# Optimization experiments

Measured on AMD Instinct MI355X. Metric: run time of the kernel, lower is better.

The kernel has to match this reference:

```python
import jax, jax.numpy as jnp
import numpy as np

N, E, FE, H, G, L, OUT = 50000, 300000, 64, 256, 256, 4, 128
BN_EPS = 1e-5


def setup_inputs() -> dict:
    key = jax.random.key(0)
    ks = jax.random.split(key, 12)
    s = 0.05
    return dict(
        x=jax.random.normal(ks[0], (N, H), jnp.float32),
        edge_index=jax.random.randint(ks[1], (2, E), 0, N, dtype=jnp.int64),
        edge_attr=jax.random.normal(ks[2], (E, FE), jnp.float32),
        batch=jnp.sort(jax.random.randint(ks[3], (N,), 0, G, dtype=jnp.int64)),
        bond_W1=jax.random.normal(ks[4], (L, FE, H), jnp.float32) * s,
        bond_b1=jnp.zeros((L, H), jnp.float32),
        bond_W2=jax.random.normal(ks[5], (L, H, H), jnp.float32) * s,
        bond_b2=jnp.zeros((L, H), jnp.float32),
        mlp_W1=jax.random.normal(ks[6], (L, H, H), jnp.float32) * s,
        mlp_b1=jnp.zeros((L, H), jnp.float32),
        mlp_W2=jax.random.normal(ks[7], (L, H, H), jnp.float32) * s,
        mlp_b2=jnp.zeros((L, H), jnp.float32),
        eps=jnp.zeros((L,), jnp.float32),
        bn_gamma=jnp.ones((L, H), jnp.float32),
        bn_beta=jnp.zeros((L, H), jnp.float32),
        fc1_W=jax.random.normal(ks[8], (L * H, H), jnp.float32) * s,
        fc1_b=jnp.zeros((H,), jnp.float32),
        fc4_W=jax.random.normal(ks[9], (H, OUT), jnp.float32) * s,
        fc4_b=jnp.zeros((OUT,), jnp.float32),
    )


def reference(x, edge_index, edge_attr, batch,
              bond_W1, bond_b1, bond_W2, bond_b2,
              mlp_W1, mlp_b1, mlp_W2, mlp_b2,
              eps, bn_gamma, bn_beta,
              fc1_W, fc1_b, fc4_W, fc4_b):
    src, dst = edge_index[0], edge_index[1]  # x_j gathered from src, scatter-add to dst
    x_lst = []
    for l in range(L):
        # bond encoder: Linear -> ReLU -> Linear on edge features [E, FE] -> [E, H]
        e = jax.nn.relu(edge_attr @ bond_W1[l] + bond_b1[l]) @ bond_W2[l] + bond_b2[l]
        # message = relu(x_j + e), aggregate = scatter-add over destination nodes
        msg = jax.nn.relu(x[src] + e)  # [E, H]
        aggr = jax.ops.segment_sum(msg, dst, num_segments=N)  # [N, H]
        h = (1.0 + eps[l]) * x + aggr
        h = jax.nn.relu(h @ mlp_W1[l] + mlp_b1[l]) @ mlp_W2[l] + mlp_b2[l]
        h = jax.nn.relu(h)
        # BatchNorm over the node dimension (training-style batch statistics)
        mu = jnp.mean(h, axis=0)
        var = jnp.var(h, axis=0)
        x = (h - mu) * jax.lax.rsqrt(var + BN_EPS) * bn_gamma[l] + bn_beta[l]
        x_lst.append(x)
    xc = jnp.concatenate(x_lst, axis=-1)  # [N, L*H]
    # global mean pool over graphs
    sums = jax.ops.segment_sum(xc, batch, num_segments=G)  # [G, L*H]
    cnts = jax.ops.segment_sum(jnp.ones((N,), xc.dtype), batch, num_segments=G)
    pooled = sums / jnp.maximum(cnts, 1.0)[:, None]
    h = jax.nn.relu(pooled @ fc1_W + fc1_b)
    # dropout p=0.5 in eval mode -> identity
    return h @ fc4_W + fc4_b  # [G, OUT]
```

## Files before the change

### kernel.cpp

```cpp
#include <hip/hip_runtime.h>

#define NN 50000
#define NE 300000
#define FEA 64
#define HD 256
#define NG 256
#define NL 4
#define OD 128
#define SCB ((NN + 255) / 256)

typedef unsigned short u16;
typedef unsigned int u32;
typedef __attribute__((ext_vector_type(8))) short short8;
typedef __attribute__((ext_vector_type(4))) short s16x4;
typedef __attribute__((ext_vector_type(4))) float f32x4;

__device__ __forceinline__ u16 f2h(float f) {
    union { _Float16 h; u16 u; } v; v.h = (_Float16)f; return v.u;
}
__device__ __forceinline__ float h2f(u16 u) {
    union { u16 u; _Float16 h; } v; v.u = u; return (float)v.h;
}

typedef const __attribute__((address_space(1))) unsigned int gas_u32;
typedef __attribute__((address_space(3))) unsigned int las_u32;
__device__ __forceinline__ void gld16(const void* g, void* l) {
    __builtin_amdgcn_global_load_lds((gas_u32*)g, (las_u32*)l, 16, 0, 0);
}

__global__ __launch_bounds__(256, 2) void edge_k(
    const u16* __restrict__ eattrS, const u16* __restrict__ W1t,
    const float* __restrict__ bb1, const u16* __restrict__ W2t,
    const float* __restrict__ bb2,
    const int* __restrict__ srcI, const int* __restrict__ dstI,
    const u16* __restrict__ xh, float* __restrict__ aggr)
{
    __shared__ __align__(16) u16 bufW[256 * 64];
    __shared__ __align__(16) u16 bufT[64 * 256];
    __shared__ int srcL[64];
    const int tid = threadIdx.x;
    const int lane = tid & 63;
    const int w = tid >> 6;
    const int q = lane >> 4, c15 = lane & 15;
    const int e0 = blockIdx.x * 64;
    const int wb = tid & ~63;

    if (tid < 64) {
        int er = e0 + tid;
        int erc = er < NE ? er : NE - 1;
        srcL[tid] = srcI[erc];
    }
#pragma unroll
    for (int it = 0; it < 2; ++it) {
        const int i = it * 256 + tid;
        const int m = i >> 3, kb = i & 7;
        int row = e0 + m; if (row > NE - 1) row = NE - 1;
        gld16(eattrS + (size_t)row * FEA + ((kb ^ (m & 7)) * 8),
              &bufT[(it * 256 + wb) * 8]);
    }
#pragma unroll
    for (int it = 0; it < 8; ++it) {
        const int i = it * 256 + tid;
        const int n = i >> 3, kb = i & 7;
        gld16(W1t + (size_t)n * FEA + ((kb ^ (n & 7)) * 8),
              &bufW[(it * 256 + wb) * 8]);
    }
    __syncthreads();

    f32x4 acc1[4][4];
#pragma unroll
    for (int i = 0; i < 4; ++i)
#pragma unroll
        for (int j = 0; j < 4; ++j) acc1[i][j] = (f32x4)0.0f;
#pragma unroll
    for (int s = 0; s < 2; ++s) {
        short8 af[4], bf[4];
#pragma unroll
        for (int t = 0; t < 4; ++t) {
            const int kga = s * 4 + q;
            const int mm = t * 16 + c15;
            af[t] = *(const short8*)&bufT[mm * 64 + ((kga ^ (mm & 7)) * 8)];
            const int nn = w * 64 + t * 16 + c15;
            bf[t] = *(const short8*)&bufW[nn * 64 + ((kga ^ (nn & 7)) * 8)];
        }
        __builtin_amdgcn_s_setprio(1);
#pragma unroll
        for (int tm = 0; tm < 4; ++tm)
#pragma unroll
            for (int tn = 0; tn < 4; ++tn)
                acc1[tm][tn] = __builtin_amdgcn_mfma_f32_16x16x32_f16(
                    bf[tm], af[tn], acc1[tm][tn], 0, 0, 0);
        __builtin_amdgcn_s_setprio(0);
    }
    __syncthreads();

    auto stageW2 = [&](int cc) {
        const int k0c = cc * 32;
        const int hB = (cc & 1) * 1024;
#pragma unroll
        for (int it = 0; it < 4; ++it) {
            const int i = it * 256 + tid;
            const int n = i >> 2, j = i & 3;
            gld16(W2t + (size_t)n * HD + k0c + ((j ^ ((n >> 1) & 3)) * 8),
                  &bufW[(hB + it * 256 + wb) * 8]);
        }
    };
    stageW2(0);

    {
#pragma unroll
        for (int tm = 0; tm < 4; ++tm) {
            const float4 b1v = *(const float4*)(bb1 + w * 64 + tm * 16 + q * 4);
            const int kb = w * 8 + tm * 2 + (q >> 1);
#pragma unroll
            for (int tn = 0; tn < 4; ++tn) {
                const int edge = tn * 16 + c15;
                s16x4 o;
#pragma unroll
                for (int r = 0; r < 4; ++r) {
                    float v = acc1[tm][tn][r] + ((const float*)&b1v)[r];
                    v = v > 0.0f ? v : 0.0f;
                    o[r] = (short)f2h(v);
                }
                *(s16x4*)((char*)bufT + edge * 512 +
                          ((kb ^ (edge & 7)) << 4) + ((q & 1) << 3)) = o;
            }
        }
    }
    __syncthreads();

    f32x4 acc2[4][4];
#pragma unroll
    for (int i = 0; i < 4; ++i)
#pragma unroll
        for (int j = 0; j < 4; ++j) acc2[i][j] = (f32x4)0.0f;
#pragma unroll
    for (int c = 0; c < 8; ++c) {
        if (c < 7) {
            stageW2(c + 1);
        } else {
#pragma unroll
            for (int it = 0; it < 4; ++it) {
                const int i = it * 256 + tid;
                const int row = i >> 5, ch = i & 31;
                gld16(xh + (size_t)srcL[row] * HD + ch * 8,
                      &bufW[(it * 256 + wb) * 8]);
            }
        }
        short8 af[4], bf[4];
        const u16* hp = &bufW[(c & 1) * 8192];
#pragma unroll
        for (int t = 0; t < 4; ++t) {
            const int mm = t * 16 + c15;
            const int kbg = c * 4 + q;
            af[t] = *(const short8*)&bufT[mm * 256 + ((kbg ^ (mm & 7)) * 8)];
            const int nn = w * 64 + t * 16 + c15;
            bf[t] = *(const short8*)&hp[nn * 32 + ((q ^ ((nn >> 1) & 3)) * 8)];
        }
        __builtin_amdgcn_s_setprio(1);
#pragma unroll
        for (int tm = 0; tm < 4; ++tm)
#pragma unroll
            for (int tn = 0; tn < 4; ++tn)
                acc2[tm][tn] = __builtin_amdgcn_mfma_f32_16x16x32_f16(
                    af[tm], bf[tn], acc2[tm][tn], 0, 0, 0);
        __builtin_amdgcn_s_setprio(0);
        __syncthreads();
    }

#pragma unroll
    for (int it = 0; it < 4; ++it) {
        const int i = 1024 + it * 256 + tid;
        const int row = i >> 5, ch = i & 31;
        gld16(xh + (size_t)srcL[row] * HD + ch * 8,
              &bufW[(1024 + it * 256 + wb) * 8]);
    }
    float b2f[4];
#pragma unroll
    for (int tn = 0; tn < 4; ++tn)
        b2f[tn] = bb2[w * 64 + tn * 16 + c15];
    __syncthreads();

#pragma unroll
    for (int tm = 0; tm < 4; ++tm) {
        const int rc = tm * 2 + (q >> 1);
#pragma unroll
        for (int tn = 0; tn < 4; ++tn) {
            const int col = w * 64 + tn * 16 + c15;
            s16x4 o;
#pragma unroll
            for (int r = 0; r < 4; ++r) {
                const int row = tm * 16 + q * 4 + r;
                float v = acc2[tm][tn][r] + b2f[tn]
                        + h2f(bufW[row * 256 + col]);
                v = v > 0.0f ? v : 0.0f;
                o[r] = (short)f2h(v);
            }
            *(s16x4*)((char*)bufT + col * 128 +
                      ((rc ^ (col & 7)) << 4) + ((q & 1) << 3)) = o;
        }
    }
    __syncthreads();

    {
        const char* bT = (const char*)bufT;
        float s = 0.0f;
        int cur = dstI[e0];
#pragma unroll
        for (int j = 0; j < 8; ++j) {
            short8 m8 = *(const short8*)(bT + tid * 128 + ((j ^ (tid & 7)) << 4));
#pragma unroll
            for (int si = 0; si < 8; ++si) {
                const int er = e0 + j * 8 + si;
                const int d = (er < NE) ? dstI[er] : -1;
                if (d != cur) {
                    if (cur >= 0 && s != 0.0f)
                        unsafeAtomicAdd(&aggr[(size_t)cur * HD + tid], s);
                    cur = d; s = 0.0f;
                }
                s += h2f((u16)m8[si]);
            }
        }
        if (cur >= 0 && s != 0.0f)
            unsafeAtomicAdd(&aggr[(size_t)cur * HD + tid], s);
    }
}

__global__ __launch_bounds__(256, 2) void node_k(
    const u16* __restrict__ xh, const float* __restrict__ aggr,
    const float* __restrict__ epsv, int l,
    const u16* __restrict__ M1t, const float* __restrict__ mb1,
    const u16* __restrict__ M2t, const float* __restrict__ mb2,
    u16* __restrict__ hb, float* __restrict__ bns, float* __restrict__ bnq)
{
    __shared__ __align__(16) u16 bufW[256 * 64];
    __shared__ __align__(16) u16 bufT[64 * 256];
    const int tid = threadIdx.x;
    const int lane = tid & 63;
    const int w = tid >> 6;
    const int q = lane >> 4, c15 = lane & 15;
    const int n0b = blockIdx.x * 64;
    const float e1 = 1.0f + epsv[l];
    const int wb = tid & ~63;

    auto stageM = [&](const u16* Mt, int cc) {
        const int k0c = cc * 32;
        const int hB = (cc & 1) * 1024;
#pragma unroll
        for (int it = 0; it < 4; ++it) {
            const int i = it * 256 + tid;
            const int n = i >> 2, j = i & 3;
            gld16(Mt + (size_t)n * HD + k0c + ((j ^ ((n >> 1) & 3)) * 8),
                  &bufW[(hB + it * 256 + wb) * 8]);
        }
    };
    stageM(M1t, 0);

#pragma unroll
    for (int it = 0; it < 8; ++it) {
        const int i = it * 256 + tid;
        const int m = i >> 5, kb = i & 31;
        int row = n0b + m; if (row > NN - 1) row = NN - 1;
        const size_t base = (size_t)row * HD + kb * 8;
        short8 xv = *(const short8*)(xh + base);
        float4 a0 = *(const float4*)(aggr + base);
        float4 a1 = *(const float4*)(aggr + base + 4);
        u16 o[8];
        o[0] = f2h(e1 * h2f((u16)xv[0]) + a0.x);
        o[1] = f2h(e1 * h2f((u16)xv[1]) + a0.y);
        o[2] = f2h(e1 * h2f((u16)xv[2]) + a0.z);
        o[3] = f2h(e1 * h2f((u16)xv[3]) + a0.w);
        o[4] = f2h(e1 * h2f((u16)xv[4]) + a1.x);
        o[5] = f2h(e1 * h2f((u16)xv[5]) + a1.y);
        o[6] = f2h(e1 * h2f((u16)xv[6]) + a1.z);
        o[7] = f2h(e1 * h2f((u16)xv[7]) + a1.w);
        *(short8*)&bufT[m * 256 + ((kb ^ (m & 7)) * 8)] = *(short8*)o;
    }
    __syncthreads();

    f32x4 acc1[4][4];
#pragma unroll
    for (int i = 0; i < 4; ++i)
#pragma unroll
        for (int j = 0; j < 4; ++j) acc1[i][j] = (f32x4)0.0f;
#pragma unroll
    for (int c = 0; c < 8; ++c) {
        if (c < 7) stageM(M1t, c + 1);
        else       stageM(M2t, 0);
        short8 af[4], bf[4];
        const u16* hp = &bufW[(c & 1) * 8192];
#pragma unroll
        for (int t = 0; t < 4; ++t) {
            const int mm = t * 16 + c15;
            const int kbg = c * 4 + q;
            af[t] = *(const short8*)&bufT[mm * 256 + ((kbg ^ (mm & 7)) * 8)];
            const int nn = w * 64 + t * 16 + c15;
            bf[t] = *(const short8*)&hp[nn * 32 + ((q ^ ((nn >> 1) & 3)) * 8)];
        }
        __builtin_amdgcn_s_setprio(1);
#pragma unroll
        for (int tm = 0; tm < 4; ++tm)
#pragma unroll
            for (int tn = 0; tn < 4; ++tn)
                acc1[tm][tn] = __builtin_amdgcn_mfma_f32_16x16x32_f16(
                    bf[tm], af[tn], acc1[tm][tn], 0, 0, 0);
        __builtin_amdgcn_s_setprio(0);
        __syncthreads();
    }

    {
#pragma unroll
        for (int tm = 0; tm < 4; ++tm) {
            const float4 b1v = *(const float4*)(mb1 + w * 64 + tm * 16 + q * 4);
            const int kb = w * 8 + tm * 2 + (q >> 1);
#pragma unroll
            for (int tn = 0; tn < 4; ++tn) {
                const int node = tn * 16 + c15;
                s16x4 o;
#pragma unroll
                for (int r = 0; r < 4; ++r) {
                    float v = acc1[tm][tn][r] + ((const float*)&b1v)[r];
                    v = v > 0.0f ? v : 0.0f;
                    o[r] = (short)f2h(v);
                }
                *(s16x4*)((char*)bufT + node * 512 +
                          ((kb ^ (node & 7)) << 4) + ((q & 1) << 3)) = o;
            }
        }
    }
    __syncthreads();

    f32x4 acc2[4][4];
#pragma unroll
    for (int i = 0; i < 4; ++i)
#pragma unroll
        for (int j = 0; j < 4; ++j) acc2[i][j] = (f32x4)0.0f;
#pragma unroll
    for (int c = 0; c < 8; ++c) {
        if (c < 7) stageM(M2t, c + 1);
        short8 af[4], bf[4];
        const u16* hp = &bufW[(c & 1) * 8192];
#pragma unroll
        for (int t = 0; t < 4; ++t) {
            const int mm = t * 16 + c15;
            const int kbg = c * 4 + q;
            af[t] = *(const short8*)&bufT[mm * 256 + ((kbg ^ (mm & 7)) * 8)];
            const int nn = w * 64 + t * 16 + c15;
            bf[t] = *(const short8*)&hp[nn * 32 + ((q ^ ((nn >> 1) & 3)) * 8)];
        }
        __builtin_amdgcn_s_setprio(1);
#pragma unroll
        for (int tm = 0; tm < 4; ++tm)
#pragma unroll
            for (int tn = 0; tn < 4; ++tn)
                acc2[tm][tn] = __builtin_amdgcn_mfma_f32_16x16x32_f16(
                    af[tm], bf[tn], acc2[tm][tn], 0, 0, 0);
        __builtin_amdgcn_s_setprio(0);
        __syncthreads();
    }

    float b2f[4];
#pragma unroll
    for (int tn = 0; tn < 4; ++tn)
        b2f[tn] = mb2[w * 64 + tn * 16 + c15];
    float ps[4] = {0, 0, 0, 0}, pq[4] = {0, 0, 0, 0};
#pragma unroll
    for (int tm = 0; tm < 4; ++tm) {
#pragma unroll
        for (int r = 0; r < 4; ++r) {
            const int grow = n0b + tm * 16 + q * 4 + r;
            if (grow < NN) {
#pragma unroll
                for (int tn = 0; tn < 4; ++tn) {
                    const int col = w * 64 + tn * 16 + c15;
                    float v = acc2[tm][tn][r] + b2f[tn];
                    v = v > 0.0f ? v : 0.0f;
                    hb[(size_t)grow * HD + col] = f2h(v);
                    ps[tn] += v; pq[tn] += v * v;
                }
            }
        }
    }
#pragma unroll
    for (int tn = 0; tn < 4; ++tn) {
        float s = ps[tn], sq = pq[tn];
        s += __shfl_down(s, 32, 64);  sq += __shfl_down(sq, 32, 64);
        s += __shfl_down(s, 16, 64);  sq += __shfl_down(sq, 16, 64);
        if (q == 0) {
            const int col = w * 64 + tn * 16 + c15;
            unsafeAtomicAdd(&bns[col], s);
            unsafeAtomicAdd(&bnq[col], sq);
        }
    }
}


__global__ void transpose_k(const float* __restrict__ in, u16* __restrict__ oh,
                            int Kw, int Nw) {
    int i = blockIdx.x * blockDim.x + threadIdx.x;
    int tot = NL * Kw * Nw;
    if (i < tot) {
        int l = i / (Kw * Nw), rem = i % (Kw * Nw);
        int k = rem / Nw, n = rem % Nw;
        oh[(size_t)l * Kw * Nw + (size_t)n * Kw + k] = f2h(in[i]);
    }
}

__global__ void cvt_k(const float* __restrict__ in, u16* __restrict__ outh, int tot) {
    int i = blockIdx.x * blockDim.x + threadIdx.x;
    if (i < tot) outh[i] = f2h(in[i]);
}

__global__ void egather_k(const float* __restrict__ eattr, const int* __restrict__ perm,
                          u16* __restrict__ eattrS) {
    int i = blockIdx.x * blockDim.x + threadIdx.x;
    if (i < NE * FEA) {
        int row = i >> 6, k = i & 63;
        eattrS[i] = f2h(eattr[(size_t)perm[row] * FEA + k]);
    }
}

__global__ void zero_layer_k(float* __restrict__ aggr, float* __restrict__ bns,
                             float* __restrict__ bnq) {
    int i = blockIdx.x * blockDim.x + threadIdx.x;
    if (i < NN * HD) aggr[i] = 0.0f;
    if (i < HD) { bns[i] = 0.0f; bnq[i] = 0.0f; }
}

__global__ void zerof_k(float* __restrict__ p, int n) {
    int i = blockIdx.x * blockDim.x + threadIdx.x;
    if (i < n) p[i] = 0.0f;
}

__global__ void bnfin_k(const float* __restrict__ bns, const float* __restrict__ bnq,
                        const float* __restrict__ gamma, const float* __restrict__ beta,
                        int l, float* __restrict__ ab) {
    int c = threadIdx.x;
    float mu = bns[c] * (1.0f / (float)NN);
    float var = bnq[c] * (1.0f / (float)NN) - mu * mu;
    if (var < 0.0f) var = 0.0f;
    float a = gamma[l * HD + c] * rsqrtf(var + 1e-5f);
    float b = beta[l * HD + c] - mu * a;
    ab[c] = a; ab[HD + c] = b;
}

__global__ void bnapply_k(const u16* __restrict__ hb, const float* __restrict__ ab,
                          const int* __restrict__ batch, u16* __restrict__ xh,
                          float* __restrict__ pooled, int l) {
    const int t = threadIdx.x;
    const int n0 = blockIdx.x * 64;
    const float a = ab[t], b = ab[HD + t];
    const int hi = (NN - n0 < 64) ? (NN - n0) : 64;
    float s = 0.0f;
    int cur = batch[n0];
    for (int r = 0; r < hi; ++r) {
        const size_t idx = (size_t)(n0 + r) * HD + t;
        float v = a * h2f(hb[idx]) + b;
        xh[idx] = f2h(v);
        const int g = batch[n0 + r];
        if (g != cur) {
            unsafeAtomicAdd(&pooled[(size_t)cur * (NL * HD) + l * HD + t], s);
            s = 0.0f; cur = g;
        }
        s += v;
    }
    unsafeAtomicAdd(&pooled[(size_t)cur * (NL * HD) + l * HD + t], s);
}


__global__ void zeroi_k(int* __restrict__ a, int n) {
    int i = blockIdx.x * blockDim.x + threadIdx.x;
    if (i < n) a[i] = 0;
}

__global__ void hist_k(const int* __restrict__ dst, int* __restrict__ hist) {
    int e = blockIdx.x * blockDim.x + threadIdx.x;
    if (e < NE) atomicAdd(&hist[dst[e]], 1);
}

__global__ void sumblk_k(const int* __restrict__ hist, int* __restrict__ psum) {
    __shared__ int red[256];
    int b = blockIdx.x, t = threadIdx.x, i = b * 256 + t;
    red[t] = (i < NN) ? hist[i] : 0;
    __syncthreads();
    for (int o = 128; o > 0; o >>= 1) {
        if (t < o) red[t] += red[t + o];
        __syncthreads();
    }
    if (t == 0) psum[b] = red[0];
}

__global__ void scanblk_k(int* __restrict__ psum) {
    __shared__ int sc[256];
    int t = threadIdx.x;
    int v = (t < SCB) ? psum[t] : 0;
    sc[t] = v; __syncthreads();
    for (int o = 1; o < 256; o <<= 1) {
        int x = (t >= o) ? sc[t - o] : 0;
        __syncthreads(); sc[t] += x; __syncthreads();
    }
    if (t < SCB) psum[t] = sc[t] - v;
}

__global__ void scanfin_k(const int* __restrict__ hist, const int* __restrict__ psum,
                          int* __restrict__ rowptr) {
    __shared__ int sc[256];
    int b = blockIdx.x, t = threadIdx.x, i = b * 256 + t;
    int v = (i < NN) ? hist[i] : 0;
    sc[t] = v; __syncthreads();
    for (int o = 1; o < 256; o <<= 1) {
        int x = (t >= o) ? sc[t - o] : 0;
        __syncthreads(); sc[t] += x; __syncthreads();
    }
    if (i < NN) rowptr[i] = psum[b] + sc[t] - v;
    if (i == NN - 1) rowptr[NN] = psum[b] + sc[t];
}

__global__ void copyi_k(const int* __restrict__ src, int* __restrict__ dst, int n) {
    int i = blockIdx.x * blockDim.x + threadIdx.x;
    if (i < n) dst[i] = src[i];
}

__global__ void scatter_k(const int* __restrict__ dst, int* __restrict__ next,
                          int* __restrict__ perm) {
    int e = blockIdx.x * blockDim.x + threadIdx.x;
    if (e < NE) {
        int p = atomicAdd(&next[dst[e]], 1);
        perm[p] = e;
    }
}

__global__ void permsd_k(const int* __restrict__ eidx, const int* __restrict__ perm,
                         int* __restrict__ srcS, int* __restrict__ dstS) {
    int i = blockIdx.x * blockDim.x + threadIdx.x;
    if (i < NE) {
        int e = perm[i];
        srcS[i] = eidx[e];
        dstS[i] = eidx[NE + e];
    }
}


__global__ void zcnt_k(int* __restrict__ cnts) {
    if (threadIdx.x < NG) cnts[threadIdx.x] = 0;
}

__global__ void count_k(const int* __restrict__ batch, int* __restrict__ cnts) {
    int i = blockIdx.x * blockDim.x + threadIdx.x;
    if (i < NN) atomicAdd(&cnts[batch[i]], 1);
}

__global__ void fc_k(const float* __restrict__ pooled, const int* __restrict__ cnts,
                     const float* __restrict__ W1, const float* __restrict__ b1,
                     const float* __restrict__ W4, const float* __restrict__ b4,
                     float* __restrict__ out) {
    __shared__ float pl[NL * HD];
    __shared__ float hm[HD];
    int g = blockIdx.x, t = threadIdx.x;
    const float inv = 1.0f / fmaxf((float)cnts[g], 1.0f);
#pragma unroll
    for (int j = 0; j < 4; ++j)
        pl[t + j * 256] = pooled[(size_t)g * 1024 + t + j * 256] * inv;
    __syncthreads();
    float a = b1[t];
    for (int k = 0; k < 1024; ++k) a += pl[k] * W1[k * 256 + t];
    hm[t] = a > 0.0f ? a : 0.0f;
    __syncthreads();
    if (t < OD) {
        float o = b4[t];
        for (int k = 0; k < 256; ++k) o += hm[k] * W4[k * OD + t];
        out[g * OD + t] = o;
    }
}


extern "C" void kernel_launch(void* const* d_in, const int* in_sizes, int n_in,
                              void* d_out, int out_size, void* d_ws, size_t ws_size,
                              hipStream_t stream) {
    const float* x_in  = (const float*)d_in[0];
    const int*   eidx  = (const int*)d_in[1];
    const float* eattr = (const float*)d_in[2];
    const int*   batch = (const int*)d_in[3];
    const float* bW1   = (const float*)d_in[4];
    const float* bb1   = (const float*)d_in[5];
    const float* bW2   = (const float*)d_in[6];
    const float* bb2   = (const float*)d_in[7];
    const float* mW1   = (const float*)d_in[8];
    const float* mb1   = (const float*)d_in[9];
    const float* mW2   = (const float*)d_in[10];
    const float* mb2   = (const float*)d_in[11];
    const float* epsv  = (const float*)d_in[12];
    const float* gamma = (const float*)d_in[13];
    const float* beta  = (const float*)d_in[14];
    const float* fc1W  = (const float*)d_in[15];
    const float* fc1b  = (const float*)d_in[16];
    const float* fc4W  = (const float*)d_in[17];
    const float* fc4b  = (const float*)d_in[18];
    float* out = (float*)d_out;
    (void)in_sizes; (void)n_in; (void)out_size; (void)ws_size;

    size_t off = 0;
    auto alloc = [&](size_t bytes) -> char* {
        char* r = (char*)d_ws + off;
        off = (off + bytes + 255) & ~(size_t)255;
        return r;
    };
    u16*   xh   = (u16*)alloc((size_t)NN * HD * 2);
    float* aggr = (float*)alloc((size_t)NN * HD * 4);
    u16*   hb   = (u16*)alloc((size_t)NN * HD * 2);
    u16*   eattrS = (u16*)alloc((size_t)NE * FEA * 2);
    u16*   W1t  = (u16*)alloc((size_t)NL * FEA * HD * 2);
    u16*   W2t  = (u16*)alloc((size_t)NL * HD * HD * 2);
    u16*   M1t  = (u16*)alloc((size_t)NL * HD * HD * 2);
    u16*   M2t  = (u16*)alloc((size_t)NL * HD * HD * 2);
    float* bns  = (float*)alloc(HD * 4);
    float* bnq  = (float*)alloc(HD * 4);
    float* ab   = (float*)alloc(2 * HD * 4);
    int*   cnts = (int*)alloc(NG * 4);
    float* pooled = (float*)alloc((size_t)NG * NL * HD * 4);
    int*   hist  = (int*)alloc((size_t)NN * 4);
    int*   psum  = (int*)alloc((size_t)SCB * 4);
    int*   rowptr = (int*)alloc((size_t)(NN + 1) * 4);
    int*   perm  = (int*)alloc((size_t)NE * 4);
    int*   srcS  = (int*)alloc((size_t)NE * 4);
    int*   dstS  = (int*)alloc((size_t)NE * 4);

    const int NEL = NN * HD;
    const int EB = (NEL + 255) / 256;
    const int NEB = (NE + 255) / 256;

    transpose_k<<<(NL * FEA * HD + 255) / 256, 256, 0, stream>>>(bW1, W1t, FEA, HD);
    transpose_k<<<(NL * HD * HD + 255) / 256, 256, 0, stream>>>(bW2, W2t, HD, HD);
    transpose_k<<<(NL * HD * HD + 255) / 256, 256, 0, stream>>>(mW1, M1t, HD, HD);
    transpose_k<<<(NL * HD * HD + 255) / 256, 256, 0, stream>>>(mW2, M2t, HD, HD);

    cvt_k<<<EB, 256, 0, stream>>>(x_in, xh, NEL);

    zeroi_k<<<(NN + 255) / 256, 256, 0, stream>>>(hist, NN);
    hist_k<<<NEB, 256, 0, stream>>>(eidx + NE, hist);
    sumblk_k<<<SCB, 256, 0, stream>>>(hist, psum);
    scanblk_k<<<1, 256, 0, stream>>>(psum);
    scanfin_k<<<SCB, 256, 0, stream>>>(hist, psum, rowptr);
    copyi_k<<<(NN + 255) / 256, 256, 0, stream>>>(rowptr, hist, NN);
    scatter_k<<<NEB, 256, 0, stream>>>(eidx + NE, hist, perm);
    permsd_k<<<NEB, 256, 0, stream>>>(eidx, perm, srcS, dstS);
    egather_k<<<(NE * FEA + 255) / 256, 256, 0, stream>>>(eattr, perm, eattrS);

    zcnt_k<<<1, 256, 0, stream>>>(cnts);
    count_k<<<(NN + 255) / 256, 256, 0, stream>>>(batch, cnts);
    zerof_k<<<(NG * NL * HD + 255) / 256, 256, 0, stream>>>(pooled, NG * NL * HD);

    const int EGB = (NE + 63) / 64;
    const int NGB = (NN + 63) / 64;

    for (int l = 0; l < NL; ++l) {
        zero_layer_k<<<EB, 256, 0, stream>>>(aggr, bns, bnq);
        edge_k<<<EGB, 256, 0, stream>>>(
            eattrS, W1t + (size_t)l * FEA * HD, bb1 + l * HD,
            W2t + (size_t)l * HD * HD, bb2 + l * HD,
            srcS, dstS, xh, aggr);
        node_k<<<NGB, 256, 0, stream>>>(
            xh, aggr, epsv, l,
            M1t + (size_t)l * HD * HD, mb1 + l * HD,
            M2t + (size_t)l * HD * HD, mb2 + l * HD,
            hb, bns, bnq);
        bnfin_k<<<1, HD, 0, stream>>>(bns, bnq, gamma, beta, l, ab);
        bnapply_k<<<NGB, 256, 0, stream>>>(hb, ab, batch, xh, pooled, l);
    }
    fc_k<<<NG, 256, 0, stream>>>(pooled, cnts, fc1W, fc1b, fc4W, fc4b, out);
}
```

Measured before the change: 1.268 ms.

## Read MFMA weight fragments directly from global memory, dropping LDS weight staging

Result: slower. 1.389 ms (+9.5%).

```diff
diff --git a/kernel.cpp b/kernel.cpp
--- a/kernel.cpp
+++ b/kernel.cpp
@@ -28,15 +28,15 @@
     __builtin_amdgcn_global_load_lds((gas_u32*)g, (las_u32*)l, 16, 0, 0);
 }
 
-__global__ __launch_bounds__(256, 2) void edge_k(
+__global__ __launch_bounds__(256, 3) void edge_k(
     const u16* __restrict__ eattrS, const u16* __restrict__ W1t,
     const float* __restrict__ bb1, const u16* __restrict__ W2t,
     const float* __restrict__ bb2,
     const int* __restrict__ srcI, const int* __restrict__ dstI,
     const u16* __restrict__ xh, float* __restrict__ aggr)
 {
-    __shared__ __align__(16) u16 bufW[256 * 64];
     __shared__ __align__(16) u16 bufT[64 * 256];
+    __shared__ __align__(16) u16 bufG[32 * 256];
     __shared__ int srcL[64];
     const int tid = threadIdx.x;
     const int lane = tid & 63;
@@ -58,14 +58,24 @@
         gld16(eattrS + (size_t)row * FEA + ((kb ^ (m & 7)) * 8),
               &bufT[(it * 256 + wb) * 8]);
     }
-#pragma unroll
-    for (int it = 0; it < 8; ++it) {
+    __syncthreads();
+
+#pragma unroll
+    for (int it = 0; it < 4; ++it) {
         const int i = it * 256 + tid;
-        const int n = i >> 3, kb = i & 7;
-        gld16(W1t + (size_t)n * FEA + ((kb ^ (n & 7)) * 8),
-              &bufW[(it * 256 + wb) * 8]);
-    }
-    __syncthreads();
+        const int row = i >> 5, ch = i & 31;
+        gld16(xh + (size_t)srcL[row] * HD + ch * 8,
+              &bufG[(it * 256 + wb) * 8]);
+    }
+
+    const u16* w1p[4];
+    const u16* w2p[4];
+#pragma unroll
+    for (int t = 0; t < 4; ++t) {
+        const int nn = w * 64 + t * 16 + c15;
+        w1p[t] = W1t + (size_t)nn * FEA + q * 8;
+        w2p[t] = W2t + (size_t)nn * HD + q * 8;
+    }
 
     f32x4 acc1[4][4];
 #pragma unroll
@@ -80,8 +90,7 @@
             const int kga = s * 4 + q;
             const int mm = t * 16 + c15;
             af[t] = *(const short8*)&bufT[mm * 64 + ((kga ^ (mm & 7)) * 8)];
-            const int nn = w * 64 + t * 16 + c15;
-            bf[t] = *(const short8*)&bufW[nn * 64 + ((kga ^ (nn & 7)) * 8)];
+            bf[t] = *(const short8*)(w1p[t] + s * 32);
         }
         __builtin_amdgcn_s_setprio(1);
 #pragma unroll
@@ -93,19 +102,6 @@
         __builtin_amdgcn_s_setprio(0);
     }
     __syncthreads();
-
-    auto stageW2 = [&](int cc) {
-        const int k0c = cc * 32;
-        const int hB = (cc & 1) * 1024;
-#pragma unroll
-        for (int it = 0; it < 4; ++it) {
-            const int i = it * 256 + tid;
-            const int n = i >> 2, j = i & 3;
-            gld16(W2t + (size_t)n * HD + k0c + ((j ^ ((n >> 1) & 3)) * 8),
-                  &bufW[(hB + it * 256 + wb) * 8]);
-        }
-    };
-    stageW2(0);
 
     {
 #pragma unroll
@@ -136,26 +132,13 @@
         for (int j = 0; j < 4; ++j) acc2[i][j] = (f32x4)0.0f;
 #pragma unroll
     for (int c = 0; c < 8; ++c) {
-        if (c < 7) {
-            stageW2(c + 1);
-        } else {
-#pragma unroll
-            for (int it = 0; it < 4; ++it) {
-                const int i = it * 256 + tid;
-                const int row = i >> 5, ch = i & 31;
-                gld16(xh + (size_t)srcL[row] * HD + ch * 8,
-                      &bufW[(it * 256 + wb) * 8]);
-            }
-        }
         short8 af[4], bf[4];
-        const u16* hp = &bufW[(c & 1) * 8192];
 #pragma unroll
         for (int t = 0; t < 4; ++t) {
             const int mm = t * 16 + c15;
             const int kbg = c * 4 + q;
             af[t] = *(const short8*)&bufT[mm * 256 + ((kbg ^ (mm & 7)) * 8)];
-            const int nn = w * 64 + t * 16 + c15;
-            bf[t] = *(const short8*)&hp[nn * 32 + ((q ^ ((nn >> 1) & 3)) * 8)];
+            bf[t] = *(const short8*)(w2p[t] + c * 32);
         }
         __builtin_amdgcn_s_setprio(1);
 #pragma unroll
@@ -165,16 +148,8 @@
                 acc2[tm][tn] = __builtin_amdgcn_mfma_f32_16x16x32_f16(
                     af[tm], bf[tn], acc2[tm][tn], 0, 0, 0);
         __builtin_amdgcn_s_setprio(0);
-        __syncthreads();
-    }
-
-#pragma unroll
-    for (int it = 0; it < 4; ++it) {
-        const int i = 1024 + it * 256 + tid;
-        const int row = i >> 5, ch = i & 31;
-        gld16(xh + (size_t)srcL[row] * HD + ch * 8,
-              &bufW[(1024 + it * 256 + wb) * 8]);
-    }
+    }
+
     float b2f[4];
 #pragma unroll
     for (int tn = 0; tn < 4; ++tn)
@@ -182,7 +157,7 @@
     __syncthreads();
 
 #pragma unroll
-    for (int tm = 0; tm < 4; ++tm) {
+    for (int tm = 0; tm < 2; ++tm) {
         const int rc = tm * 2 + (q >> 1);
 #pragma unroll
         for (int tn = 0; tn < 4; ++tn) {
@@ -192,7 +167,37 @@
             for (int r = 0; r < 4; ++r) {
                 const int row = tm * 16 + q * 4 + r;
                 float v = acc2[tm][tn][r] + b2f[tn]
-                        + h2f(bufW[row * 256 + col]);
+                        + h2f(bufG[row * 256 + col]);
+                v = v > 0.0f ? v : 0.0f;
+                o[r] = (short)f2h(v);
+            }
+            *(s16x4*)((char*)bufT + col * 128 +
+                      ((rc ^ (col & 7)) << 4) + ((q & 1) << 3)) = o;
+        }
+    }
+    __syncthreads();
+
+#pragma unroll
+    for (int it = 0; it < 4; ++it) {
+        const int i = it * 256 + tid;
+        const int row = 32 + (i >> 5), ch = i & 31;
+        gld16(xh + (size_t)srcL[row] * HD + ch * 8,
+              &bufG[(it * 256 + wb) * 8]);
+    }
+    __syncthreads();
+
+#pragma unroll
+    for (int tm = 2; tm < 4; ++tm) {
+        const int rc = tm * 2 + (q >> 1);
+#pragma unroll
+        for (int tn = 0; tn < 4; ++tn) {
+            const int col = w * 64 + tn * 16 + c15;
+            s16x4 o;
+#pragma unroll
+            for (int r = 0; r < 4; ++r) {
+                const int rowG = (tm - 2) * 16 + q * 4 + r;
+                float v = acc2[tm][tn][r] + b2f[tn]
+                        + h2f(bufG[rowG * 256 + col]);
                 v = v > 0.0f ? v : 0.0f;
                 o[r] = (short)f2h(v);
             }
@@ -226,14 +231,13 @@
     }
 }
 
-__global__ __launch_bounds__(256, 2) void node_k(
+__global__ __launch_bounds__(256, 4) void node_k(
     const u16* __restrict__ xh, const float* __restrict__ aggr,
     const float* __restrict__ epsv, int l,
     const u16* __restrict__ M1t, const float* __restrict__ mb1,
     const u16* __restrict__ M2t, const float* __restrict__ mb2,
     u16* __restrict__ hb, float* __restrict__ bns, float* __restrict__ bnq)
 {
-    __shared__ __align__(16) u16 bufW[256 * 64];
     __shared__ __align__(16) u16 bufT[64 * 256];
     const int tid = threadIdx.x;
     const int lane = tid & 63;
@@ -241,20 +245,15 @@
     const int q = lane >> 4, c15 = lane & 15;
     const int n0b = blockIdx.x * 64;
     const float e1 = 1.0f + epsv[l];
-    const int wb = tid & ~63;
-
-    auto stageM = [&](const u16* Mt, int cc) {
-        const int k0c = cc * 32;
-        const int hB = (cc & 1) * 1024;
-#pragma unroll
-        for (int it = 0; it < 4; ++it) {
-            const int i = it * 256 + tid;
-            const int n = i >> 2, j = i & 3;
-            gld16(Mt + (size_t)n * HD + k0c + ((j ^ ((n >> 1) & 3)) * 8),
-                  &bufW[(hB + it * 256 + wb) * 8]);
-        }
-    };
-    stageM(M1t, 0);
+
+    const u16* m1p[4];
+    const u16* m2p[4];
+#pragma unroll
+    for (int t = 0; t < 4; ++t) {
+        const int nn = w * 64 + t * 16 + c15;
+        m1p[t] = M1t + (size_t)nn * HD + q * 8;
+        m2p[t] = M2t + (size_t)nn * HD + q * 8;
+    }
 
 #pragma unroll
     for (int it = 0; it < 8; ++it) {
@@ -285,17 +284,13 @@
         for (int j = 0; j < 4; ++j) acc1[i][j] = (f32x4)0.0f;
 #pragma unroll
     for (int c = 0; c < 8; ++c) {
-        if (c < 7) stageM(M1t, c + 1);
-        else       stageM(M2t, 0);
         short8 af[4], bf[4];
-        const u16* hp = &bufW[(c & 1) * 8192];
 #pragma unroll
         for (int t = 0; t < 4; ++t) {
             const int mm = t * 16 + c15;
             const int kbg = c * 4 + q;
             af[t] = *(const short8*)&bufT[mm * 256 + ((kbg ^ (mm & 7)) * 8)];
-            const int nn = w * 64 + t * 16 + c15;
-            bf[t] = *(const short8*)&hp[nn * 32 + ((q ^ ((nn >> 1) & 3)) * 8)];
+            bf[t] = *(const short8*)(m1p[t] + c * 32);
         }
         __builtin_amdgcn_s_setprio(1);
 #pragma unroll
@@ -305,8 +300,8 @@
                 acc1[tm][tn] = __builtin_amdgcn_mfma_f32_16x16x32_f16(
                     bf[tm], af[tn], acc1[tm][tn], 0, 0, 0);
         __builtin_amdgcn_s_setprio(0);
-        __syncthreads();
-    }
+    }
+    __syncthreads();
 
     {
 #pragma unroll
@@ -337,16 +332,13 @@
         for (int j = 0; j < 4; ++j) acc2[i][j] = (f32x4)0.0f;
 #pragma unroll
     for (int c = 0; c < 8; ++c) {
-        if (c < 7) stageM(M2t, c + 1);
         short8 af[4], bf[4];
-        const u16* hp = &bufW[(c & 1) * 8192];
 #pragma unroll
         for (int t = 0; t < 4; ++t) {
             const int mm = t * 16 + c15;
             const int kbg = c * 4 + q;
             af[t] = *(const short8*)&bufT[mm * 256 + ((kbg ^ (mm & 7)) * 8)];
-            const int nn = w * 64 + t * 16 + c15;
-            bf[t] = *(const short8*)&hp[nn * 32 + ((q ^ ((nn >> 1) & 3)) * 8)];
+            bf[t] = *(const short8*)(m2p[t] + c * 32);
         }
         __builtin_amdgcn_s_setprio(1);
 #pragma unroll
@@ -356,7 +348,6 @@
                 acc2[tm][tn] = __builtin_amdgcn_mfma_f32_16x16x32_f16(
                     af[tm], bf[tn], acc2[tm][tn], 0, 0, 0);
         __builtin_amdgcn_s_setprio(0);
-        __syncthreads();
     }
 
     float b2f[4];
@@ -420,10 +411,10 @@
     }
 }
 
-__global__ void zero_layer_k(float* __restrict__ aggr, float* __restrict__ bns,
+__global__ void zero_layer_k(float4* __restrict__ aggr4, float* __restrict__ bns,
                              float* __restrict__ bnq) {
     int i = blockIdx.x * blockDim.x + threadIdx.x;
-    if (i < NN * HD) aggr[i] = 0.0f;
+    if (i < (NN * HD) / 4) aggr4[i] = make_float4(0.f, 0.f, 0.f, 0.f);
     if (i < HD) { bns[i] = 0.0f; bnq[i] = 0.0f; }
 }
 
@@ -627,6 +618,7 @@
 
     const int NEL = NN * HD;
     const int EB = (NEL + 255) / 256;
+    const int EB4 = (NEL / 4 + 255) / 256;
     const int NEB = (NE + 255) / 256;
 
     transpose_k<<<(NL * FEA * HD + 255) / 256, 256, 0, stream>>>(bW1, W1t, FEA, HD);
@@ -654,7 +646,7 @@
     const int NGB = (NN + 63) / 64;
 
     for (int l = 0; l < NL; ++l) {
-        zero_layer_k<<<EB, 256, 0, stream>>>(aggr, bns, bnq);
+        zero_layer_k<<<EB4, 256, 0, stream>>>((float4*)aggr, bns, bnq);
         edge_k<<<EGB, 256, 0, stream>>>(
             eattrS, W1t + (size_t)l * FEA * HD, bb1 + l * HD,
             W2t + (size_t)l * HD * HD, bb2 + l * HD,
```

## Split edge and node GEMM tiles across eight waves and vectorize aggr zeroing

Applied to the files above, without the earlier changes.

Result: slower. 1.346 ms (+6.1%).

```diff
diff --git a/kernel.cpp b/kernel.cpp
--- a/kernel.cpp
+++ b/kernel.cpp
@@ -28,7 +28,7 @@
     __builtin_amdgcn_global_load_lds((gas_u32*)g, (las_u32*)l, 16, 0, 0);
 }
 
-__global__ __launch_bounds__(256, 2) void edge_k(
+__global__ __launch_bounds__(512, 4) void edge_k(
     const u16* __restrict__ eattrS, const u16* __restrict__ W1t,
     const float* __restrict__ bb1, const u16* __restrict__ W2t,
     const float* __restrict__ bb2,
@@ -50,42 +50,44 @@
         int erc = er < NE ? er : NE - 1;
         srcL[tid] = srcI[erc];
     }
-#pragma unroll
-    for (int it = 0; it < 2; ++it) {
-        const int i = it * 256 + tid;
-        const int m = i >> 3, kb = i & 7;
+    {
+        const int m = tid >> 3, kb = tid & 7;
         int row = e0 + m; if (row > NE - 1) row = NE - 1;
         gld16(eattrS + (size_t)row * FEA + ((kb ^ (m & 7)) * 8),
-              &bufT[(it * 256 + wb) * 8]);
-    }
-#pragma unroll
-    for (int it = 0; it < 8; ++it) {
-        const int i = it * 256 + tid;
+              &bufT[wb * 8]);
+    }
+#pragma unroll
+    for (int it = 0; it < 4; ++it) {
+        const int i = it * 512 + tid;
         const int n = i >> 3, kb = i & 7;
         gld16(W1t + (size_t)n * FEA + ((kb ^ (n & 7)) * 8),
-              &bufW[(it * 256 + wb) * 8]);
-    }
-    __syncthreads();
-
-    f32x4 acc1[4][4];
-#pragma unroll
-    for (int i = 0; i < 4; ++i)
+              &bufW[(it * 512 + wb) * 8]);
+    }
+    __syncthreads();
+
+    f32x4 acc1[2][4];
+#pragma unroll
+    for (int i = 0; i < 2; ++i)
 #pragma unroll
         for (int j = 0; j < 4; ++j) acc1[i][j] = (f32x4)0.0f;
 #pragma unroll
     for (int s = 0; s < 2; ++s) {
-        short8 af[4], bf[4];
+        short8 af[4], bf[2];
 #pragma unroll
         for (int t = 0; t < 4; ++t) {
             const int kga = s * 4 + q;
             const int mm = t * 16 + c15;
             af[t] = *(const short8*)&bufT[mm * 64 + ((kga ^ (mm & 7)) * 8)];
-            const int nn = w * 64 + t * 16 + c15;
+        }
+#pragma unroll
+        for (int t = 0; t < 2; ++t) {
+            const int kga = s * 4 + q;
+            const int nn = w * 32 + t * 16 + c15;
             bf[t] = *(const short8*)&bufW[nn * 64 + ((kga ^ (nn & 7)) * 8)];
         }
         __builtin_amdgcn_s_setprio(1);
 #pragma unroll
-        for (int tm = 0; tm < 4; ++tm)
+        for (int tm = 0; tm < 2; ++tm)
 #pragma unroll
             for (int tn = 0; tn < 4; ++tn)
                 acc1[tm][tn] = __builtin_amdgcn_mfma_f32_16x16x32_f16(
@@ -98,20 +100,20 @@
         const int k0c = cc * 32;
         const int hB = (cc & 1) * 1024;
 #pragma unroll
-        for (int it = 0; it < 4; ++it) {
-            const int i = it * 256 + tid;
+        for (int it = 0; it < 2; ++it) {
+            const int i = it * 512 + tid;
             const int n = i >> 2, j = i & 3;
             gld16(W2t + (size_t)n * HD + k0c + ((j ^ ((n >> 1) & 3)) * 8),
-                  &bufW[(hB + it * 256 + wb) * 8]);
+                  &bufW[(hB + it * 512 + wb) * 8]);
         }
     };
     stageW2(0);
 
     {
 #pragma unroll
-        for (int tm = 0; tm < 4; ++tm) {
-            const float4 b1v = *(const float4*)(bb1 + w * 64 + tm * 16 + q * 4);
-            const int kb = w * 8 + tm * 2 + (q >> 1);
+        for (int tm = 0; tm < 2; ++tm) {
+            const float4 b1v = *(const float4*)(bb1 + w * 32 + tm * 16 + q * 4);
+            const int kb = w * 4 + tm * 2 + (q >> 1);
 #pragma unroll
             for (int tn = 0; tn < 4; ++tn) {
                 const int edge = tn * 16 + c15;
@@ -129,39 +131,42 @@
     }
     __syncthreads();
 
-    f32x4 acc2[4][4];
+    f32x4 acc2[4][2];
 #pragma unroll
     for (int i = 0; i < 4; ++i)
 #pragma unroll
-        for (int j = 0; j < 4; ++j) acc2[i][j] = (f32x4)0.0f;
+        for (int j = 0; j < 2; ++j) acc2[i][j] = (f32x4)0.0f;
 #pragma unroll
     for (int c = 0; c < 8; ++c) {
         if (c < 7) {
             stageW2(c + 1);
         } else {
 #pragma unroll
-            for (int it = 0; it < 4; ++it) {
-                const int i = it * 256 + tid;
+            for (int it = 0; it < 2; ++it) {
+                const int i = it * 512 + tid;
                 const int row = i >> 5, ch = i & 31;
                 gld16(xh + (size_t)srcL[row] * HD + ch * 8,
-                      &bufW[(it * 256 + wb) * 8]);
+                      &bufW[(it * 512 + wb) * 8]);
             }
         }
-        short8 af[4], bf[4];
+        short8 af[4], bf[2];
         const u16* hp = &bufW[(c & 1) * 8192];
 #pragma unroll
         for (int t = 0; t < 4; ++t) {
             const int mm = t * 16 + c15;
             const int kbg = c * 4 + q;
             af[t] = *(const short8*)&bufT[mm * 256 + ((kbg ^ (mm & 7)) * 8)];
-            const int nn = w * 64 + t * 16 + c15;
+        }
+#pragma unroll
+        for (int t = 0; t < 2; ++t) {
+            const int nn = w * 32 + t * 16 + c15;
             bf[t] = *(const short8*)&hp[nn * 32 + ((q ^ ((nn >> 1) & 3)) * 8)];
         }
         __builtin_amdgcn_s_setprio(1);
 #pragma unroll
         for (int tm = 0; tm < 4; ++tm)
 #pragma unroll
-            for (int tn = 0; tn < 4; ++tn)
+            for (int tn = 0; tn < 2; ++tn)
                 acc2[tm][tn] = __builtin_amdgcn_mfma_f32_16x16x32_f16(
                     af[tm], bf[tn], acc2[tm][tn], 0, 0, 0);
         __builtin_amdgcn_s_setprio(0);
@@ -169,24 +174,24 @@
     }
 
 #pragma unroll
-    for (int it = 0; it < 4; ++it) {
-        const int i = 1024 + it * 256 + tid;
+    for (int it = 0; it < 2; ++it) {
+        const int i = 1024 + it * 512 + tid;
         const int row = i >> 5, ch = i & 31;
         gld16(xh + (size_t)srcL[row] * HD + ch * 8,
-              &bufW[(1024 + it * 256 + wb) * 8]);
-    }
-    float b2f[4];
-#pragma unroll
-    for (int tn = 0; tn < 4; ++tn)
-        b2f[tn] = bb2[w * 64 + tn * 16 + c15];
+              &bufW[(1024 + it * 512 + wb) * 8]);
+    }
+    float b2f[2];
+#pragma unroll
+    for (int tn = 0; tn < 2; ++tn)
+        b2f[tn] = bb2[w * 32 + tn * 16 + c15];
     __syncthreads();
 
 #pragma unroll
     for (int tm = 0; tm < 4; ++tm) {
         const int rc = tm * 2 + (q >> 1);
 #pragma unroll
-        for (int tn = 0; tn < 4; ++tn) {
-            const int col = w * 64 + tn * 16 + c15;
+        for (int tn = 0; tn < 2; ++tn) {
+            const int col = w * 32 + tn * 16 + c15;
             s16x4 o;
 #pragma unroll
             for (int r = 0; r < 4; ++r) {
@@ -204,29 +209,33 @@
 
     {
         const char* bT = (const char*)bufT;
+        const int half = tid >> 8;
+        const int col = tid & 255;
+        const int base = e0 + half * 32;
         float s = 0.0f;
-        int cur = dstI[e0];
-#pragma unroll
-        for (int j = 0; j < 8; ++j) {
-            short8 m8 = *(const short8*)(bT + tid * 128 + ((j ^ (tid & 7)) << 4));
+        int cur = (base < NE) ? dstI[base] : -1;
+#pragma unroll
+        for (int j = 0; j < 4; ++j) {
+            const int jj = half * 4 + j;
+            short8 m8 = *(const short8*)(bT + col * 128 + ((jj ^ (col & 7)) << 4));
 #pragma unroll
             for (int si = 0; si < 8; ++si) {
-                const int er = e0 + j * 8 + si;
+                const int er = base + j * 8 + si;
                 const int d = (er < NE) ? dstI[er] : -1;
                 if (d != cur) {
                     if (cur >= 0 && s != 0.0f)
-                        unsafeAtomicAdd(&aggr[(size_t)cur * HD + tid], s);
+                        unsafeAtomicAdd(&aggr[(size_t)cur * HD + col], s);
                     cur = d; s = 0.0f;
                 }
                 s += h2f((u16)m8[si]);
             }
         }
         if (cur >= 0 && s != 0.0f)
-            unsafeAtomicAdd(&aggr[(size_t)cur * HD + tid], s);
-    }
-}
-
-__global__ __launch_bounds__(256, 2) void node_k(
+            unsafeAtomicAdd(&aggr[(size_t)cur * HD + col], s);
+    }
+}
+
+__global__ __launch_bounds__(512, 4) void node_k(
     const u16* __restrict__ xh, const float* __restrict__ aggr,
     const float* __restrict__ epsv, int l,
     const u16* __restrict__ M1t, const float* __restrict__ mb1,
@@ -247,18 +256,18 @@
         const int k0c = cc * 32;
         const int hB = (cc & 1) * 1024;
 #pragma unroll
-        for (int it = 0; it < 4; ++it) {
-            const int i = it * 256 + tid;
+        for (int it = 0; it < 2; ++it) {
+            const int i = it * 512 + tid;
             const int n = i >> 2, j = i & 3;
             gld16(Mt + (size_t)n * HD + k0c + ((j ^ ((n >> 1) & 3)) * 8),
-                  &bufW[(hB + it * 256 + wb) * 8]);
+                  &bufW[(hB + it * 512 + wb) * 8]);
         }
     };
     stageM(M1t, 0);
 
 #pragma unroll
-    for (int it = 0; it < 8; ++it) {
-        const int i = it * 256 + tid;
+    for (int it = 0; it < 4; ++it) {
+        const int i = it * 512 + tid;
         const int m = i >> 5, kb = i & 31;
         int row = n0b + m; if (row > NN - 1) row = NN - 1;
         const size_t base = (size_t)row * HD + kb * 8;
@@ -278,28 +287,31 @@
     }
     __syncthreads();
 
-    f32x4 acc1[4][4];
-#pragma unroll
-    for (int i = 0; i < 4; ++i)
+    f32x4 acc1[2][4];
+#pragma unroll
+    for (int i = 0; i < 2; ++i)
 #pragma unroll
         for (int j = 0; j < 4; ++j) acc1[i][j] = (f32x4)0.0f;
 #pragma unroll
     for (int c = 0; c < 8; ++c) {
         if (c < 7) stageM(M1t, c + 1);
         else       stageM(M2t, 0);
-        short8 af[4], bf[4];
+        short8 af[4], bf[2];
         const u16* hp = &bufW[(c & 1) * 8192];
 #pragma unroll
         for (int t = 0; t < 4; ++t) {
             const int mm = t * 16 + c15;
             const int kbg = c * 4 + q;
             af[t] = *(const short8*)&bufT[mm * 256 + ((kbg ^ (mm & 7)) * 8)];
-            const int nn = w * 64 + t * 16 + c15;
+        }
+#pragma unroll
+        for (int t = 0; t < 2; ++t) {
+            const int nn = w * 32 + t * 16 + c15;
             bf[t] = *(const short8*)&hp[nn * 32 + ((q ^ ((nn >> 1) & 3)) * 8)];
         }
         __builtin_amdgcn_s_setprio(1);
 #pragma unroll
-        for (int tm = 0; tm < 4; ++tm)
+        for (int tm = 0; tm < 2; ++tm)
 #pragma unroll
             for (int tn = 0; tn < 4; ++tn)
                 acc1[tm][tn] = __builtin_amdgcn_mfma_f32_16x16x32_f16(
@@ -310,9 +322,9 @@
 
     {
 #pragma unroll
-        for (int tm = 0; tm < 4; ++tm) {
-            const float4 b1v = *(const float4*)(mb1 + w * 64 + tm * 16 + q * 4);
-            const int kb = w * 8 + tm * 2 + (q >> 1);
+        for (int tm = 0; tm < 2; ++tm) {
+            const float4 b1v = *(const float4*)(mb1 + w * 32 + tm * 16 + q * 4);
+            const int kb = w * 4 + tm * 2 + (q >> 1);
 #pragma unroll
             for (int tn = 0; tn < 4; ++tn) {
                 const int node = tn * 16 + c15;
@@ -330,40 +342,43 @@
     }
     __syncthreads();
 
-    f32x4 acc2[4][4];
+    f32x4 acc2[4][2];
 #pragma unroll
     for (int i = 0; i < 4; ++i)
 #pragma unroll
-        for (int j = 0; j < 4; ++j) acc2[i][j] = (f32x4)0.0f;
+        for (int j = 0; j < 2; ++j) acc2[i][j] = (f32x4)0.0f;
 #pragma unroll
     for (int c = 0; c < 8; ++c) {
         if (c < 7) stageM(M2t, c + 1);
-        short8 af[4], bf[4];
+        short8 af[4], bf[2];
         const u16* hp = &bufW[(c & 1) * 8192];
 #pragma unroll
         for (int t = 0; t < 4; ++t) {
             const int mm = t * 16 + c15;
             const int kbg = c * 4 + q;
             af[t] = *(const short8*)&bufT[mm * 256 + ((kbg ^ (mm & 7)) * 8)];
-            const int nn = w * 64 + t * 16 + c15;
+        }
+#pragma unroll
+        for (int t = 0; t < 2; ++t) {
+            const int nn = w * 32 + t * 16 + c15;
             bf[t] = *(const short8*)&hp[nn * 32 + ((q ^ ((nn >> 1) & 3)) * 8)];
         }
         __builtin_amdgcn_s_setprio(1);
 #pragma unroll
         for (int tm = 0; tm < 4; ++tm)
 #pragma unroll
-            for (int tn = 0; tn < 4; ++tn)
+            for (int tn = 0; tn < 2; ++tn)
                 acc2[tm][tn] = __builtin_amdgcn_mfma_f32_16x16x32_f16(
                     af[tm], bf[tn], acc2[tm][tn], 0, 0, 0);
         __builtin_amdgcn_s_setprio(0);
         __syncthreads();
     }
 
-    float b2f[4];
-#pragma unroll
-    for (int tn = 0; tn < 4; ++tn)
-        b2f[tn] = mb2[w * 64 + tn * 16 + c15];
-    float ps[4] = {0, 0, 0, 0}, pq[4] = {0, 0, 0, 0};
+    float b2f[2];
+#pragma unroll
+    for (int tn = 0; tn < 2; ++tn)
+        b2f[tn] = mb2[w * 32 + tn * 16 + c15];
+    float ps[2] = {0, 0}, pq[2] = {0, 0};
 #pragma unroll
     for (int tm = 0; tm < 4; ++tm) {
 #pragma unroll
@@ -371,8 +386,8 @@
             const int grow = n0b + tm * 16 + q * 4 + r;
             if (grow < NN) {
 #pragma unroll
-                for (int tn = 0; tn < 4; ++tn) {
-                    const int col = w * 64 + tn * 16 + c15;
+                for (int tn = 0; tn < 2; ++tn) {
+                    const int col = w * 32 + tn * 16 + c15;
                     float v = acc2[tm][tn][r] + b2f[tn];
                     v = v > 0.0f ? v : 0.0f;
                     hb[(size_t)grow * HD + col] = f2h(v);
@@ -382,12 +397,12 @@
         }
     }
 #pragma unroll
-    for (int tn = 0; tn < 4; ++tn) {
+    for (int tn = 0; tn < 2; ++tn) {
         float s = ps[tn], sq = pq[tn];
         s += __shfl_down(s, 32, 64);  sq += __shfl_down(sq, 32, 64);
         s += __shfl_down(s, 16, 64);  sq += __shfl_down(sq, 16, 64);
         if (q == 0) {
-            const int col = w * 64 + tn * 16 + c15;
+            const int col = w * 32 + tn * 16 + c15;
             unsafeAtomicAdd(&bns[col], s);
             unsafeAtomicAdd(&bnq[col], sq);
         }
@@ -420,10 +435,10 @@
     }
 }
 
-__global__ void zero_layer_k(float* __restrict__ aggr, float* __restrict__ bns,
+__global__ void zero_layer_k(float4* __restrict__ aggr4, float* __restrict__ bns,
                              float* __restrict__ bnq) {
     int i = blockIdx.x * blockDim.x + threadIdx.x;
-    if (i < NN * HD) aggr[i] = 0.0f;
+    if (i < (NN * HD) / 4) aggr4[i] = make_float4(0.f, 0.f, 0.f, 0.f);
     if (i < HD) { bns[i] = 0.0f; bnq[i] = 0.0f; }
 }
 
@@ -627,6 +642,7 @@
 
     const int NEL = NN * HD;
     const int EB = (NEL + 255) / 256;
+    const int EB4 = (NEL / 4 + 255) / 256;
     const int NEB = (NE + 255) / 256;
 
     transpose_k<<<(NL * FEA * HD + 255) / 256, 256, 0, stream>>>(bW1, W1t, FEA, HD);
@@ -654,12 +670,12 @@
     const int NGB = (NN + 63) / 64;
 
     for (int l = 0; l < NL; ++l) {
-        zero_layer_k<<<EB, 256, 0, stream>>>(aggr, bns, bnq);
-        edge_k<<<EGB, 256, 0, stream>>>(
+        zero_layer_k<<<EB4, 256, 0, stream>>>((float4*)aggr, bns, bnq);
+        edge_k<<<EGB, 512, 0, stream>>>(
             eattrS, W1t + (size_t)l * FEA * HD, bb1 + l * HD,
             W2t + (size_t)l * HD * HD, bb2 + l * HD,
             srcS, dstS, xh, aggr);
-        node_k<<<NGB, 256, 0, stream>>>(
+        node_k<<<NGB, 512, 0, stream>>>(
             xh, aggr, epsv, l,
             M1t + (size_t)l * HD * HD, mb1 + l * HD,
             M2t + (size_t)l * HD * HD, mb2 + l * HD,
```
